# Kernel optimization log

Measured on AMD Instinct MI355X. Metric: run time of the kernel, lower is better.

The kernel has to match this reference:

```python
import jax, jax.numpy as jnp
import numpy as np

N_HEAD = 12
SEQ = 4096
D_MODEL = 768


def setup_inputs() -> dict:
    key = jax.random.key(0)
    ks = jax.random.split(key, 5)
    tokens = jax.random.normal(ks[0], (SEQ, D_MODEL), dtype=jnp.float32)
    # GPT-2 causal mask buffer: lower-triangular ones, shape [1,1,n_ctx,n_ctx]
    attn_bias = jnp.tril(jnp.ones((SEQ, SEQ), dtype=jnp.float32))[None, None]
    c_attn_weight = jax.random.normal(ks[1], (D_MODEL, 3 * D_MODEL), dtype=jnp.float32) * 0.02
    c_attn_bias = jax.random.normal(ks[2], (3 * D_MODEL,), dtype=jnp.float32) * 0.02
    c_proj_weight = jax.random.normal(ks[3], (D_MODEL, D_MODEL), dtype=jnp.float32) * 0.02
    c_proj_bias = jax.random.normal(ks[4], (D_MODEL,), dtype=jnp.float32) * 0.02
    return {
        "tokens": tokens,
        "attn_bias": attn_bias,
        "c_attn_weight": c_attn_weight,
        "c_attn_bias": c_attn_bias,
        "c_proj_weight": c_proj_weight,
        "c_proj_bias": c_proj_bias,
    }


def reference(tokens, attn_bias, c_attn_weight, c_attn_bias, c_proj_weight, c_proj_bias):
    S, D = tokens.shape
    H = N_HEAD
    hd = D // H
    qkv = tokens @ c_attn_weight + c_attn_bias          # [S, 3D]
    q, k, v = jnp.split(qkv, 3, axis=1)                 # each [S, D]
    q = q.reshape(S, H, hd).transpose(1, 0, 2)          # [H, S, hd]
    kh = k.reshape(S, H, hd).transpose(1, 2, 0)         # [H, hd, S] (key pre-transposed)
    vh = v.reshape(S, H, hd).transpose(1, 0, 2)         # [H, S, hd]
    w = jnp.einsum('hqd,hdk->hqk', q, kh) / jnp.sqrt(jnp.float32(hd))  # [H, S, S]
    nd, ns = S, S
    b = attn_bias[0, :, ns - nd:ns, :ns]                # [1, S, S], broadcasts over heads
    w = w * b - 1e10 * (1.0 - b)
    p = jax.nn.softmax(w, axis=-1)
    a = jnp.einsum('hqk,hkd->hqd', p, vh)               # [H, S, hd]
    a = a.transpose(1, 0, 2).reshape(S, D)              # merge heads
    out = a @ c_proj_weight + c_proj_bias               # [S, D]
    return out
```

## Files before the change

kernel.cpp:

```cpp
#include <hip/hip_runtime.h>

typedef __attribute__((ext_vector_type(8))) short s8v;
typedef __attribute__((ext_vector_type(4))) float f32x4;
typedef __attribute__((ext_vector_type(16))) float f32x16;
typedef __attribute__((ext_vector_type(4))) unsigned short u16x4;
typedef __attribute__((ext_vector_type(4))) unsigned int u32x4;
typedef __attribute__((ext_vector_type(4))) _Float16 h16x4;

#define SEQ 4096
#define DM  768
#define NH  12
#define HD  64
#define QSCL 0.18033688f
#define FOFF 8.0f

__device__ __forceinline__ unsigned short f2bf(float f) {
  union { float f; unsigned int u; } v; v.f = f;
  unsigned int r = v.u + 0x7fffu + ((v.u >> 16) & 1u);
  return (unsigned short)(r >> 16);
}

__device__ __forceinline__ unsigned int cvtpk(float lo, float hi) {
  unsigned int r;
  asm("v_cvt_pk_bf16_f32 %0, %1, %2" : "=v"(r) : "v"(lo), "v"(hi));
  return r;
}

__device__ __forceinline__ void gload16(const void* g, void* l) {
  __builtin_amdgcn_global_load_lds((const __attribute__((address_space(1))) void*)g,
                                   (__attribute__((address_space(3))) void*)l, 16, 0, 0);
}

__global__ __launch_bounds__(256) void k_cast(const float* __restrict__ in,
                                              unsigned short* __restrict__ out) {
  int i = (blockIdx.x * 256 + threadIdx.x) * 4;
  float4 v = *reinterpret_cast<const float4*>(in + i);
  u16x4 o;
  o.x = f2bf(v.x); o.y = f2bf(v.y); o.z = f2bf(v.z); o.w = f2bf(v.w);
  *reinterpret_cast<u16x4*>(out + i) = o;
}

__global__ __launch_bounds__(256) void k_transpose_cast(const float* __restrict__ in,
                                                        unsigned short* __restrict__ out,
                                                        int K, int N) {
  __shared__ float tile[32][33];
  int k0 = blockIdx.x * 32, n0 = blockIdx.y * 32;
  int tr = threadIdx.x >> 5, tc = threadIdx.x & 31;
#pragma unroll
  for (int i = 0; i < 4; i++)
    tile[i * 8 + tr][tc] = in[(k0 + i * 8 + tr) * N + n0 + tc];
  __syncthreads();
#pragma unroll
  for (int i = 0; i < 4; i++)
    out[(n0 + i * 8 + tr) * K + k0 + tc] = f2bf(tile[tc][i * 8 + tr]);
}

template<int MODE>
__global__ __launch_bounds__(256) void k_gemm(
    const unsigned short* __restrict__ A, const unsigned short* __restrict__ BT,
    const float* __restrict__ bias,
    unsigned short* __restrict__ Oq, unsigned short* __restrict__ Ok,
    unsigned short* __restrict__ Ov, float* __restrict__ Of) {
  __shared__ unsigned short As[128 * 32];
  __shared__ unsigned short Bs[128 * 32];
  const int tid = threadIdx.x;
  const int lane = tid & 63;
  const int w = tid >> 6;
  const int wm = w >> 1, wn = w & 1;
  const int l15 = lane & 15, l4 = lane >> 4;
  const int m0 = blockIdx.x * 128, n0 = blockIdx.y * 128;

  f32x4 acc[4][4] = {};

  int srow[2], skc[2];
#pragma unroll
  for (int j = 0; j < 2; j++) {
    int slot = j * 256 + tid;
    srow[j] = slot >> 2;
    skc[j] = (slot & 3) ^ ((srow[j] >> 1) & 3);
  }
  const int ldsb0 = (tid & ~63) * 16;
  const int ldsb1 = (256 + (tid & ~63)) * 16;

  for (int k0 = 0; k0 < DM; k0 += 32) {
    gload16(A + (m0 + srow[0]) * DM + k0 + skc[0] * 8, (char*)As + ldsb0);
    gload16(A + (m0 + srow[1]) * DM + k0 + skc[1] * 8, (char*)As + ldsb1);
    gload16(BT + (n0 + srow[0]) * DM + k0 + skc[0] * 8, (char*)Bs + ldsb0);
    gload16(BT + (n0 + srow[1]) * DM + k0 + skc[1] * 8, (char*)Bs + ldsb1);
    __syncthreads();
    s8v af[4], bfr[4];
#pragma unroll
    for (int i = 0; i < 4; i++) {
      int ra = wm * 64 + i * 16 + l15;
      int ca = (l4 ^ ((ra >> 1) & 3)) * 8;
      af[i] = *reinterpret_cast<const s8v*>(&As[ra * 32 + ca]);
      int rb = wn * 64 + i * 16 + l15;
      int cb = (l4 ^ ((rb >> 1) & 3)) * 8;
      bfr[i] = *reinterpret_cast<const s8v*>(&Bs[rb * 32 + cb]);
    }
#pragma unroll
    for (int mi = 0; mi < 4; mi++)
#pragma unroll
      for (int nj = 0; nj < 4; nj++)
        acc[mi][nj] = __builtin_amdgcn_mfma_f32_16x16x32_bf16(af[mi], bfr[nj], acc[mi][nj], 0, 0, 0);
    __syncthreads();
  }

#pragma unroll
  for (int nj = 0; nj < 4; nj++) {
    const int col = n0 + wn * 64 + nj * 16 + l15;
    const float bv = bias[col];
#pragma unroll
    for (int mi = 0; mi < 4; mi++) {
      const int rowb = m0 + wm * 64 + mi * 16 + l4 * 4;
      if (MODE == 0) {
        if (col < 768) {
#pragma unroll
          for (int r = 0; r < 4; r++)
            Oq[(rowb + r) * DM + col] = f2bf((acc[mi][nj][r] + bv) * QSCL);
        } else if (col < 1536) {
#pragma unroll
          for (int r = 0; r < 4; r++)
            Ok[(rowb + r) * DM + (col - 768)] = f2bf(acc[mi][nj][r] + bv);
        } else {
          u16x4 pk;
#pragma unroll
          for (int r = 0; r < 4; r++)
            pk[r] = f2bf(acc[mi][nj][r] + bv);
          *reinterpret_cast<u16x4*>(&Ov[(col - 1536) * SEQ + rowb]) = pk;
        }
      } else {
#pragma unroll
        for (int r = 0; r < 4; r++)
          Of[(rowb + r) * DM + col] = acc[mi][nj][r] + bv;
      }
    }
  }
}

__global__ __launch_bounds__(256, 4) void k_attn(
    const unsigned short* __restrict__ Qb, const unsigned short* __restrict__ Kb,
    const unsigned short* __restrict__ Vt, _Float16* __restrict__ Opart,
    float* __restrict__ lw) {
  __shared__ unsigned short Ks[2][64 * 64];
  __shared__ unsigned short Vs[2][64 * 64];
  const int tid = threadIdx.x;
  const int lane = tid & 63;
  const int w = tid >> 6;
  const int l31 = lane & 31, lh = lane >> 5;
  const int bid = blockIdx.x;
  const int s = bid & 3;
  const int b2 = bid >> 2;
  const int head = b2 % NH;
  const int qt = 31 - (b2 / NH);
  const int q0w = qt * 128 + w * 32;
  const int ntiles = 2 * qt + 2;

  const unsigned short* const Kh = Kb + head * HD;
  const unsigned short* const Vh = Vt + head * HD * SEQ;

  int srow[2], scol[2];
#pragma unroll
  for (int j = 0; j < 2; j++) {
    int c = j * 256 + tid;
    srow[j] = c >> 3;
    scol[j] = ((c & 7) ^ (srow[j] & 7)) * 8;
  }
  const int ldsoff0 = (tid & ~63) * 16;
  const int ldsoff1 = 4096 + (tid & ~63) * 16;

  s8v aq[4];
#pragma unroll
  for (int kc = 0; kc < 4; kc++)
    aq[kc] = *reinterpret_cast<const s8v*>(
        &Qb[(q0w + l31) * DM + head * HD + kc * 16 + lh * 8]);

  const int x7 = l31 & 7;
  const int rbase = l31 * 128;

  f32x16 O0 = {}, O1 = {};
  float lsum = 0.f;

  if (s < ntiles) {
    const int kb0 = s * 64;
    gload16(Kh + (kb0 + srow[0]) * DM + scol[0], (char*)Ks[0] + ldsoff0);
    gload16(Kh + (kb0 + srow[1]) * DM + scol[1], (char*)Ks[0] + ldsoff1);
    gload16(Vh + srow[0] * SEQ + kb0 + scol[0], (char*)Vs[0] + ldsoff0);
    gload16(Vh + srow[1] * SEQ + kb0 + scol[1], (char*)Vs[0] + ldsoff1);
    __asm__ volatile("s_waitcnt vmcnt(0)" ::: "memory");
  }
  __syncthreads();

  for (int t = s; t < ntiles; t += 4) {
    const int cur = ((t - s) >> 2) & 1;
    if (t + 4 < ntiles) {
      const int kb2 = (t + 4) * 64;
      const int nxt = cur ^ 1;
      gload16(Kh + (kb2 + srow[0]) * DM + scol[0], (char*)Ks[nxt] + ldsoff0);
      gload16(Kh + (kb2 + srow[1]) * DM + scol[1], (char*)Ks[nxt] + ldsoff1);
      gload16(Vh + srow[0] * SEQ + kb2 + scol[0], (char*)Vs[nxt] + ldsoff0);
      gload16(Vh + srow[1] * SEQ + kb2 + scol[1], (char*)Vs[nxt] + ldsoff1);
    }
    const int kb = t * 64;
    if (kb <= q0w + 31) {
      const char* const kbuf = (const char*)Ks[cur];
      const char* const vbuf = (const char*)Vs[cur];
      f32x16 z0 = {}, z1 = {};
#pragma unroll
      for (int kc = 0; kc < 4; kc++) {
        const int so = ((kc * 2 + lh) ^ x7) << 4;
        const s8v k0 = *reinterpret_cast<const s8v*>(kbuf + rbase + so);
        const s8v k1 = *reinterpret_cast<const s8v*>(kbuf + 4096 + rbase + so);
        z0 = __builtin_amdgcn_mfma_f32_32x32x16_bf16(k0, aq[kc], z0, 0, 0, 0);
        z1 = __builtin_amdgcn_mfma_f32_32x32x16_bf16(k1, aq[kc], z1, 0, 0, 0);
      }
      if (kb + 63 > q0w) {
        const int qm = q0w + l31 - kb - 4 * lh;
#pragma unroll
        for (int r = 0; r < 16; r++) {
          const int koff = (r & 3) + 8 * (r >> 2);
          z0[r] = (koff > qm) ? -1e30f : z0[r];
          z1[r] = (koff + 32 > qm) ? -1e30f : z1[r];
        }
      }
      float sacc = 0.f;
#pragma unroll
      for (int r = 0; r < 16; r++) { z0[r] = exp2f(z0[r] - FOFF); sacc += z0[r]; }
#pragma unroll
      for (int r = 0; r < 16; r++) { z1[r] = exp2f(z1[r] - FOFF); sacc += z1[r]; }
      lsum += sacc;
      s8v pf[4];
#define PACKKC(V, base, dst)                                                 \
      {                                                                      \
        unsigned int A0 = cvtpk(V[base + 0], V[base + 1]);                   \
        unsigned int B0 = cvtpk(V[base + 2], V[base + 3]);                   \
        unsigned int A1 = cvtpk(V[base + 4], V[base + 5]);                   \
        unsigned int B1 = cvtpk(V[base + 6], V[base + 7]);                   \
        asm("v_permlane32_swap_b32 %0, %1" : "+v"(A0), "+v"(A1));            \
        asm("v_permlane32_swap_b32 %0, %1" : "+v"(B0), "+v"(B1));            \
        u32x4 q_ = {A0, B0, A1, B1};                                         \
        dst = __builtin_bit_cast(s8v, q_);                                   \
      }
      PACKKC(z0, 0, pf[0]);
      PACKKC(z0, 8, pf[1]);
      PACKKC(z1, 0, pf[2]);
      PACKKC(z1, 8, pf[3]);
#undef PACKKC
#pragma unroll
      for (int kc = 0; kc < 4; kc++) {
        const int so = ((kc * 2 + lh) ^ x7) << 4;
        const s8v v0 = *reinterpret_cast<const s8v*>(vbuf + rbase + so);
        const s8v v1 = *reinterpret_cast<const s8v*>(vbuf + 4096 + rbase + so);
        O0 = __builtin_amdgcn_mfma_f32_32x32x16_bf16(v0, pf[kc], O0, 0, 0, 0);
        O1 = __builtin_amdgcn_mfma_f32_32x32x16_bf16(v1, pf[kc], O1, 0, 0, 0);
      }
    }
    __asm__ volatile("s_waitcnt vmcnt(0)" ::: "memory");
    __syncthreads();
  }

  lsum += __shfl_xor(lsum, 32);
  _Float16* const op = Opart + (size_t)s * SEQ * DM + (size_t)(q0w + l31) * DM +
                       head * HD + 4 * lh;
#pragma unroll
  for (int k = 0; k < 4; k++) {
    h16x4 o0h, o1h;
#pragma unroll
    for (int r = 0; r < 4; r++) {
      o0h[r] = (_Float16)O0[k * 4 + r];
      o1h[r] = (_Float16)O1[k * 4 + r];
    }
    *reinterpret_cast<h16x4*>(op + 8 * k) = o0h;
    *reinterpret_cast<h16x4*>(op + 32 + 8 * k) = o1h;
  }
  if (lh == 0)
    lw[(s * NH + head) * SEQ + q0w + l31] = lsum;
}

__global__ __launch_bounds__(256) void k_merge(const _Float16* __restrict__ Opart,
                                               const float* __restrict__ lw,
                                               unsigned short* __restrict__ attn) {
  const int idx = blockIdx.x * 256 + threadIdx.x;
  const int e4 = idx * 4;
  const int row = e4 / DM;
  const int col = e4 - row * DM;
  const int head = col >> 6;
  const float l0 = lw[(0 * NH + head) * SEQ + row];
  const float l1 = lw[(1 * NH + head) * SEQ + row];
  const float l2 = lw[(2 * NH + head) * SEQ + row];
  const float l3 = lw[(3 * NH + head) * SEQ + row];
  const float rl = 1.f / (l0 + l1 + l2 + l3);
  const size_t SD = (size_t)SEQ * DM;
  const h16x4 o0 = *reinterpret_cast<const h16x4*>(Opart + e4);
  const h16x4 o1 = *reinterpret_cast<const h16x4*>(Opart + SD + e4);
  const h16x4 o2 = *reinterpret_cast<const h16x4*>(Opart + 2 * SD + e4);
  const h16x4 o3 = *reinterpret_cast<const h16x4*>(Opart + 3 * SD + e4);
  u16x4 pk;
#pragma unroll
  for (int j = 0; j < 4; j++)
    pk[j] = f2bf(((float)o0[j] + (float)o1[j] + (float)o2[j] + (float)o3[j]) * rl);
  *reinterpret_cast<u16x4*>(attn + e4) = pk;
}

extern "C" void kernel_launch(void* const* d_in, const int* in_sizes, int n_in,
                              void* d_out, int out_size, void* d_ws, size_t ws_size,
                              hipStream_t stream) {
  (void)in_sizes; (void)n_in; (void)out_size; (void)ws_size;
  const float* tokens = (const float*)d_in[0];
  const float* wqkv  = (const float*)d_in[2];
  const float* bqkv  = (const float*)d_in[3];
  const float* wproj = (const float*)d_in[4];
  const float* bproj = (const float*)d_in[5];
  float* out = (float*)d_out;

  unsigned short* tok    = (unsigned short*)d_ws;
  unsigned short* wqkvT  = tok + 4096 * 768;
  unsigned short* wprojT = wqkvT + 2304 * 768;
  unsigned short* Qb     = wprojT + 768 * 768;
  unsigned short* Kb     = Qb + 4096 * 768;
  unsigned short* Vt     = Kb + 4096 * 768;
  unsigned short* attn   = Vt + 768 * 4096;
  _Float16* Opart = (_Float16*)(attn + 4096 * 768);
  float* lw = (float*)(Opart + 4 * 4096 * 768);

  k_cast<<<3072, 256, 0, stream>>>(tokens, tok);
  k_transpose_cast<<<dim3(24, 72), 256, 0, stream>>>(wqkv, wqkvT, 768, 2304);
  k_transpose_cast<<<dim3(24, 24), 256, 0, stream>>>(wproj, wprojT, 768, 768);
  k_gemm<0><<<dim3(32, 18), 256, 0, stream>>>(tok, wqkvT, bqkv, Qb, Kb, Vt, nullptr);
  k_attn<<<1536, 256, 0, stream>>>(Qb, Kb, Vt, Opart, lw);
  k_merge<<<3072, 256, 0, stream>>>(Opart, lw, attn);
  k_gemm<1><<<dim3(32, 6), 256, 0, stream>>>(attn, wprojT, bproj, nullptr, nullptr, nullptr, out);
}
```

Baseline: 109.9 us.

## Fuse prep kernels, fold softmax offset into MFMA init, add setprio

Merges the token cast and the two weight transpose-casts into one launch, removing two kernel launches. In the attention loop, the QK accumulator now starts at -FOFF, so the subtraction before exp2 goes away. The row sum is accumulated as paired float2 values, and the K/V global offsets are advanced incrementally instead of recomputed each tile. s_setprio is raised around the MFMA blocks to favour matrix issue across waves. The masked value of -1e30 plus the offset still underflows to zero, so results should be unchanged.

```diff
diff --git a/kernel.cpp b/kernel.cpp
--- a/kernel.cpp
+++ b/kernel.cpp
@@ -1,6 +1,7 @@
 #include <hip/hip_runtime.h>
 
 typedef __attribute__((ext_vector_type(8))) short s8v;
+typedef __attribute__((ext_vector_type(2))) float f32x2;
 typedef __attribute__((ext_vector_type(4))) float f32x4;
 typedef __attribute__((ext_vector_type(16))) float f32x16;
 typedef __attribute__((ext_vector_type(4))) unsigned short u16x4;
@@ -31,28 +32,35 @@
                                    (__attribute__((address_space(3))) void*)l, 16, 0, 0);
 }
 
-__global__ __launch_bounds__(256) void k_cast(const float* __restrict__ in,
-                                              unsigned short* __restrict__ out) {
-  int i = (blockIdx.x * 256 + threadIdx.x) * 4;
-  float4 v = *reinterpret_cast<const float4*>(in + i);
-  u16x4 o;
-  o.x = f2bf(v.x); o.y = f2bf(v.y); o.z = f2bf(v.z); o.w = f2bf(v.w);
-  *reinterpret_cast<u16x4*>(out + i) = o;
-}
-
-__global__ __launch_bounds__(256) void k_transpose_cast(const float* __restrict__ in,
-                                                        unsigned short* __restrict__ out,
-                                                        int K, int N) {
+__global__ __launch_bounds__(256) void k_prep(
+    const float* __restrict__ tokens, const float* __restrict__ wqkv,
+    const float* __restrict__ wproj, unsigned short* __restrict__ tok,
+    unsigned short* __restrict__ wqkvT, unsigned short* __restrict__ wprojT) {
   __shared__ float tile[32][33];
-  int k0 = blockIdx.x * 32, n0 = blockIdx.y * 32;
-  int tr = threadIdx.x >> 5, tc = threadIdx.x & 31;
+  const int b = blockIdx.x;
+  const int tid = threadIdx.x;
+  if (b < 3072) {
+    int i = (b * 256 + tid) * 4;
+    float4 v = *reinterpret_cast<const float4*>(tokens + i);
+    u16x4 o;
+    o.x = f2bf(v.x); o.y = f2bf(v.y); o.z = f2bf(v.z); o.w = f2bf(v.w);
+    *reinterpret_cast<u16x4*>(tok + i) = o;
+    return;
+  }
+  const float* in;
+  unsigned short* out;
+  int idx, N;
+  if (b < 4800) { idx = b - 3072; in = wqkv;  out = wqkvT;  N = 2304; }
+  else          { idx = b - 4800; in = wproj; out = wprojT; N = 768;  }
+  const int k0 = (idx % 24) * 32, n0 = (idx / 24) * 32;
+  const int tr = tid >> 5, tc = tid & 31;
 #pragma unroll
   for (int i = 0; i < 4; i++)
     tile[i * 8 + tr][tc] = in[(k0 + i * 8 + tr) * N + n0 + tc];
   __syncthreads();
 #pragma unroll
   for (int i = 0; i < 4; i++)
-    out[(n0 + i * 8 + tr) * K + k0 + tc] = f2bf(tile[tc][i * 8 + tr]);
+    out[(n0 + i * 8 + tr) * 768 + k0 + tc] = f2bf(tile[tc][i * 8 + tr]);
 }
 
 template<int MODE>
@@ -168,6 +176,10 @@
   }
   const int ldsoff0 = (tid & ~63) * 16;
   const int ldsoff1 = 4096 + (tid & ~63) * 16;
+  int koff0 = (s * 64 + srow[0]) * DM + scol[0];
+  int koff1 = (s * 64 + srow[1]) * DM + scol[1];
+  int voff0 = srow[0] * SEQ + s * 64 + scol[0];
+  int voff1 = srow[1] * SEQ + s * 64 + scol[1];
 
   s8v aq[4];
 #pragma unroll
@@ -182,30 +194,35 @@
   float lsum = 0.f;
 
   if (s < ntiles) {
-    const int kb0 = s * 64;
-    gload16(Kh + (kb0 + srow[0]) * DM + scol[0], (char*)Ks[0] + ldsoff0);
-    gload16(Kh + (kb0 + srow[1]) * DM + scol[1], (char*)Ks[0] + ldsoff1);
-    gload16(Vh + srow[0] * SEQ + kb0 + scol[0], (char*)Vs[0] + ldsoff0);
-    gload16(Vh + srow[1] * SEQ + kb0 + scol[1], (char*)Vs[0] + ldsoff1);
+    gload16(Kh + koff0, (char*)Ks[0] + ldsoff0);
+    gload16(Kh + koff1, (char*)Ks[0] + ldsoff1);
+    gload16(Vh + voff0, (char*)Vs[0] + ldsoff0);
+    gload16(Vh + voff1, (char*)Vs[0] + ldsoff1);
     __asm__ volatile("s_waitcnt vmcnt(0)" ::: "memory");
   }
   __syncthreads();
+  koff0 += 256 * DM; koff1 += 256 * DM;
+  voff0 += 256;      voff1 += 256;
 
   for (int t = s; t < ntiles; t += 4) {
     const int cur = ((t - s) >> 2) & 1;
     if (t + 4 < ntiles) {
-      const int kb2 = (t + 4) * 64;
       const int nxt = cur ^ 1;
-      gload16(Kh + (kb2 + srow[0]) * DM + scol[0], (char*)Ks[nxt] + ldsoff0);
-      gload16(Kh + (kb2 + srow[1]) * DM + scol[1], (char*)Ks[nxt] + ldsoff1);
-      gload16(Vh + srow[0] * SEQ + kb2 + scol[0], (char*)Vs[nxt] + ldsoff0);
-      gload16(Vh + srow[1] * SEQ + kb2 + scol[1], (char*)Vs[nxt] + ldsoff1);
-    }
+      gload16(Kh + koff0, (char*)Ks[nxt] + ldsoff0);
+      gload16(Kh + koff1, (char*)Ks[nxt] + ldsoff1);
+      gload16(Vh + voff0, (char*)Vs[nxt] + ldsoff0);
+      gload16(Vh + voff1, (char*)Vs[nxt] + ldsoff1);
+    }
+    koff0 += 256 * DM; koff1 += 256 * DM;
+    voff0 += 256;      voff1 += 256;
     const int kb = t * 64;
     if (kb <= q0w + 31) {
       const char* const kbuf = (const char*)Ks[cur];
       const char* const vbuf = (const char*)Vs[cur];
-      f32x16 z0 = {}, z1 = {};
+      f32x16 z0, z1;
+#pragma unroll
+      for (int r = 0; r < 16; r++) { z0[r] = -FOFF; z1[r] = -FOFF; }
+      __builtin_amdgcn_s_setprio(1);
 #pragma unroll
       for (int kc = 0; kc < 4; kc++) {
         const int so = ((kc * 2 + lh) ^ x7) << 4;
@@ -214,6 +231,7 @@
         z0 = __builtin_amdgcn_mfma_f32_32x32x16_bf16(k0, aq[kc], z0, 0, 0, 0);
         z1 = __builtin_amdgcn_mfma_f32_32x32x16_bf16(k1, aq[kc], z1, 0, 0, 0);
       }
+      __builtin_amdgcn_s_setprio(0);
       if (kb + 63 > q0w) {
         const int qm = q0w + l31 - kb - 4 * lh;
 #pragma unroll
@@ -223,12 +241,20 @@
           z1[r] = (koff + 32 > qm) ? -1e30f : z1[r];
         }
       }
-      float sacc = 0.f;
-#pragma unroll
-      for (int r = 0; r < 16; r++) { z0[r] = exp2f(z0[r] - FOFF); sacc += z0[r]; }
-#pragma unroll
-      for (int r = 0; r < 16; r++) { z1[r] = exp2f(z1[r] - FOFF); sacc += z1[r]; }
-      lsum += sacc;
+      f32x2 sa = {0.f, 0.f}, sb = {0.f, 0.f};
+#pragma unroll
+      for (int r = 0; r < 8; r++) {
+        z0[2 * r] = exp2f(z0[2 * r]);
+        z0[2 * r + 1] = exp2f(z0[2 * r + 1]);
+        f32x2 e0; e0[0] = z0[2 * r]; e0[1] = z0[2 * r + 1];
+        sa += e0;
+        z1[2 * r] = exp2f(z1[2 * r]);
+        z1[2 * r + 1] = exp2f(z1[2 * r + 1]);
+        f32x2 e1; e1[0] = z1[2 * r]; e1[1] = z1[2 * r + 1];
+        sb += e1;
+      }
+      sa += sb;
+      lsum += sa[0] + sa[1];
       s8v pf[4];
 #define PACKKC(V, base, dst)                                                 \
       {                                                                      \
@@ -246,6 +272,7 @@
       PACKKC(z1, 0, pf[2]);
       PACKKC(z1, 8, pf[3]);
 #undef PACKKC
+      __builtin_amdgcn_s_setprio(1);
 #pragma unroll
       for (int kc = 0; kc < 4; kc++) {
         const int so = ((kc * 2 + lh) ^ x7) << 4;
@@ -254,6 +281,7 @@
         O0 = __builtin_amdgcn_mfma_f32_32x32x16_bf16(v0, pf[kc], O0, 0, 0, 0);
         O1 = __builtin_amdgcn_mfma_f32_32x32x16_bf16(v1, pf[kc], O1, 0, 0, 0);
       }
+      __builtin_amdgcn_s_setprio(0);
     }
     __asm__ volatile("s_waitcnt vmcnt(0)" ::: "memory");
     __syncthreads();
@@ -323,9 +351,7 @@
   _Float16* Opart = (_Float16*)(attn + 4096 * 768);
   float* lw = (float*)(Opart + 4 * 4096 * 768);
 
-  k_cast<<<3072, 256, 0, stream>>>(tokens, tok);
-  k_transpose_cast<<<dim3(24, 72), 256, 0, stream>>>(wqkv, wqkvT, 768, 2304);
-  k_transpose_cast<<<dim3(24, 24), 256, 0, stream>>>(wproj, wprojT, 768, 768);
+  k_prep<<<5376, 256, 0, stream>>>(tokens, wqkv, wproj, tok, wqkvT, wprojT);
   k_gemm<0><<<dim3(32, 18), 256, 0, stream>>>(tok, wqkvT, bqkv, Qb, Kb, Vt, nullptr);
   k_attn<<<1536, 256, 0, stream>>>(Qb, Kb, Vt, Opart, lw);
   k_merge<<<3072, 256, 0, stream>>>(Opart, lw, attn);
```

New measurement: 103.3 us. 1.06x faster.
